# Kernel tuning notes

Hardware: AMD Instinct MI355X
Metric: run time of the kernel (lower is better)

The kernel has to match this reference:

```python
import jax, jax.numpy as jnp
import numpy as np

N_TOKENS = 8192
DIM = 7168
N_EXPERTS = 256
TOPK = 8
N_GROUPS = 8
TOPK_GROUPS = 4
ROUTE_SCALE = 2.5


def setup_inputs() -> dict:
    key = jax.random.key(0)
    k1, k2, k3 = jax.random.split(key, 3)
    x = jax.random.normal(k1, (N_TOKENS, DIM), jnp.float32)
    token_mask = jnp.ones((N_TOKENS,), jnp.bool_)
    weight = jax.random.normal(k2, (N_EXPERTS, DIM), jnp.float32) * 0.02
    bias = jax.random.normal(k3, (N_EXPERTS,), jnp.float32) * 0.01
    return {"x": x, "token_mask": token_mask, "weight": weight, "bias": bias}


def reference(x, token_mask, weight, bias):
    # Router logits -> sigmoid scores (DeepSeek-V3 style gate)
    N = x.shape[0]
    scores = jax.nn.sigmoid(jnp.einsum('nd,ed->ne', x, weight))  # [N, E]
    original_scores = scores
    # bias-corrected scores used only for expert selection
    s = scores + bias  # [N, E]
    # group-limited routing: pick TOPK_GROUPS groups by sum of top-2 scores per group
    sg = s.reshape(N, N_GROUPS, N_EXPERTS // N_GROUPS)
    group_scores = jax.lax.top_k(sg, 2)[0].sum(axis=-1)  # [N, G]
    group_idx = jax.lax.top_k(group_scores, TOPK_GROUPS)[1]  # [N, topk_groups]
    mask = jnp.zeros((N, N_GROUPS), s.dtype).at[jnp.arange(N)[:, None], group_idx].set(1.0)
    masked = (sg * mask[:, :, None]).reshape(N, N_EXPERTS)
    # global top-k over group-masked, bias-corrected scores
    idx = jax.lax.top_k(masked, TOPK)[1]  # [N, TOPK] int32
    # routing weights come from the ORIGINAL (un-biased) scores
    weights = jnp.take_along_axis(original_scores, idx, axis=1)  # [N, TOPK]
    # sigmoid score_func: renormalize then scale
    weights = weights / weights.sum(axis=-1, keepdims=True)
    weights = weights * ROUTE_SCALE
    return weights.astype(x.dtype), idx
```

## Files before the change

kernel.cpp:

```cpp
#include <hip/hip_runtime.h>
#include <math.h>

#define NT 8192
#define DIM 7168
#define NE 256

#define BM 64
#define BN 64
#define BK 16

__global__ __launch_bounds__(256) void gate_gemm_f64(const float* __restrict__ x,
                                                     const float* __restrict__ w,
                                                     double* __restrict__ scores) {
    __shared__ double As[BK][BM];
    __shared__ double Bs[BK][BN];
    const int eb = blockIdx.x;
    const int mb = blockIdx.y;
    const int t  = (int)threadIdx.x;
    const int lrow = t >> 2;
    const int kq   = (t & 3) << 2;
    const int ty = t >> 4;
    const int tx = t & 15;

    const float* ag = x + (size_t)(mb * BM + lrow) * DIM + kq;
    const float* bg = w + (size_t)(eb * BN + lrow) * DIM + kq;

    double acc[4][4];
    #pragma unroll
    for (int i = 0; i < 4; ++i)
        #pragma unroll
        for (int j = 0; j < 4; ++j) acc[i][j] = 0.0;

    float4 av = *(const float4*)ag;
    float4 bv = *(const float4*)bg;

    for (int kb = 0; kb < DIM; kb += BK) {
        __syncthreads();
        As[kq + 0][lrow] = (double)av.x; As[kq + 1][lrow] = (double)av.y;
        As[kq + 2][lrow] = (double)av.z; As[kq + 3][lrow] = (double)av.w;
        Bs[kq + 0][lrow] = (double)bv.x; Bs[kq + 1][lrow] = (double)bv.y;
        Bs[kq + 2][lrow] = (double)bv.z; Bs[kq + 3][lrow] = (double)bv.w;
        __syncthreads();
        if (kb + BK < DIM) {
            av = *(const float4*)(ag + kb + BK);
            bv = *(const float4*)(bg + kb + BK);
        }
        #pragma unroll
        for (int kk = 0; kk < BK; ++kk) {
            double ar[4], br[4];
            #pragma unroll
            for (int i = 0; i < 4; ++i) ar[i] = As[kk][i * 16 + ty];
            #pragma unroll
            for (int j = 0; j < 4; ++j) br[j] = Bs[kk][j * 16 + tx];
            #pragma unroll
            for (int i = 0; i < 4; ++i)
                #pragma unroll
                for (int j = 0; j < 4; ++j)
                    acc[i][j] = fma(ar[i], br[j], acc[i][j]);
        }
    }
    #pragma unroll
    for (int i = 0; i < 4; ++i) {
        const int m = mb * BM + i * 16 + ty;
        #pragma unroll
        for (int j = 0; j < 4; ++j) {
            const double s = 1.0 / (1.0 + exp(-acc[i][j]));
            scores[(size_t)m * NE + eb * BN + j * 16 + tx] = s;
        }
    }
}

__global__ __launch_bounds__(256) void gate_route_f64(const double* __restrict__ scores,
                                                      const float* __restrict__ bias,
                                                      float* __restrict__ out) {
    const int t = (int)threadIdx.x;
    const int lane = t & 63;
    const int token = blockIdx.x * 4 + (t >> 6);

    const double4 sc4 = *(const double4*)&scores[(size_t)token * NE + lane * 4];
    const float4 bi4 = *(const float4*)&bias[lane * 4];
    const double orig[4] = {sc4.x, sc4.y, sc4.z, sc4.w};
    const double sb[4] = {orig[0] + (double)bi4.x, orig[1] + (double)bi4.y,
                          orig[2] + (double)bi4.z, orig[3] + (double)bi4.w};

    const double m1 = fmax(sb[0], sb[1]), m2 = fmin(sb[0], sb[1]);
    const double m3 = fmax(sb[2], sb[3]), m4 = fmin(sb[2], sb[3]);
    double hi = fmax(m1, m3);
    double lo = fmax(fmin(m1, m3), fmax(m2, m4));
    #pragma unroll
    for (int off = 1; off < 8; off <<= 1) {
        const double oh = __shfl_xor(hi, off);
        const double ol = __shfl_xor(lo, off);
        const double nhi = fmax(hi, oh);
        const double nlo = fmax(fmin(hi, oh), fmax(lo, ol));
        hi = nhi; lo = nlo;
    }
    const double gsum = hi + lo;
    const int g = lane >> 3;

    int rank = 0;
    #pragma unroll
    for (int j = 0; j < 8; ++j) {
        const double gj = __shfl(gsum, j * 8);
        rank += (gj > gsum) || (gj == gsum && j < g);
    }
    const bool sel = rank < 4;

    double mv[4];
    #pragma unroll
    for (int i = 0; i < 4; ++i) mv[i] = sel ? sb[i] : 0.0;

    double wsel[8];
    int isel[8];
    double wsum = 0.0;
    #pragma unroll
    for (int r = 0; r < 8; ++r) {
        double v = mv[0]; int ii = 0;
        if (mv[1] > v) { v = mv[1]; ii = 1; }
        if (mv[2] > v) { v = mv[2]; ii = 2; }
        if (mv[3] > v) { v = mv[3]; ii = 3; }
        int idx = lane * 4 + ii;
        #pragma unroll
        for (int off = 1; off < 64; off <<= 1) {
            const double ov = __shfl_xor(v, off);
            const int    oi = __shfl_xor(idx, off);
            if (ov > v || (ov == v && oi < idx)) { v = ov; idx = oi; }
        }
        const int owner = idx >> 2, slot = idx & 3;
        const double os = (slot == 0) ? orig[0] : (slot == 1) ? orig[1]
                        : (slot == 2) ? orig[2] : orig[3];
        const double ow = __shfl(os, owner);
        wsel[r] = ow; isel[r] = idx; wsum += ow;
        if (lane == owner) {
            if      (slot == 0) mv[0] = -INFINITY;
            else if (slot == 1) mv[1] = -INFINITY;
            else if (slot == 2) mv[2] = -INFINITY;
            else                mv[3] = -INFINITY;
        }
    }

    if (lane == 0) {
        const double scale = 2.5 / wsum;
        #pragma unroll
        for (int r = 0; r < 8; ++r) {
            out[(size_t)token * 8 + r] = (float)(wsel[r] * scale);
            out[(size_t)NT * 8 + (size_t)token * 8 + r] = (float)isel[r];
        }
    }
}

extern "C" void kernel_launch(void* const* d_in, const int* in_sizes, int n_in,
                              void* d_out, int out_size, void* d_ws, size_t ws_size,
                              hipStream_t stream) {
    const float* x    = (const float*)d_in[0];
    const float* w    = (const float*)d_in[2];
    const float* bias = (const float*)d_in[3];
    float* out     = (float*)d_out;
    double* scores = (double*)d_ws;

    dim3 gGemm(NE / BN, NT / BM);
    gate_gemm_f64<<<gGemm, 256, 0, stream>>>(x, w, scores);
    gate_route_f64<<<NT / 4, 256, 0, stream>>>(scores, bias, out);
}
```

Measured before the change: 1.285 ms.

## Pre-transpose gate weights to f64 and read them via uniform broadcast loads

```diff
diff --git a/kernel.cpp b/kernel.cpp
--- a/kernel.cpp
+++ b/kernel.cpp
@@ -5,69 +5,78 @@
 #define DIM 7168
 #define NE 256
 
-#define BM 64
-#define BN 64
+#define TB 256
+#define TN 16
 #define BK 16
 
+
+__global__ __launch_bounds__(256) void wt_transpose(const float* __restrict__ w,
+                                                    double* __restrict__ wt) {
+    __shared__ float tile[32][33];
+    const int kb = blockIdx.x * 32;
+    const int eb = blockIdx.y * 32;
+    const int tx = (int)threadIdx.x & 31;
+    const int ty = (int)threadIdx.x >> 5;
+    #pragma unroll
+    for (int r = 0; r < 4; ++r)
+        tile[ty + r * 8][tx] = w[(size_t)(eb + ty + r * 8) * DIM + kb + tx];
+    __syncthreads();
+    #pragma unroll
+    for (int r = 0; r < 4; ++r)
+        wt[(size_t)(kb + ty + r * 8) * NE + eb + tx] = (double)tile[tx][ty + r * 8];
+}
+
 __global__ __launch_bounds__(256) void gate_gemm_f64(const float* __restrict__ x,
-                                                     const float* __restrict__ w,
+                                                     const double* __restrict__ wt,
                                                      double* __restrict__ scores) {
-    __shared__ double As[BK][BM];
-    __shared__ double Bs[BK][BN];
-    const int eb = blockIdx.x;
-    const int mb = blockIdx.y;
-    const int t  = (int)threadIdx.x;
-    const int lrow = t >> 2;
-    const int kq   = (t & 3) << 2;
-    const int ty = t >> 4;
-    const int tx = t & 15;
+    __shared__ double As[BK][TB];
+    const int tbk = blockIdx.x;
+    const int ebk = blockIdx.y;
+    const int t = (int)threadIdx.x;
+    const int ts = t >> 2;
+    const int kc = (t & 3) << 2;
 
-    const float* ag = x + (size_t)(mb * BM + lrow) * DIM + kq;
-    const float* bg = w + (size_t)(eb * BN + lrow) * DIM + kq;
+    const float* xg = x + (size_t)(tbk * TB) * DIM;
 
-    double acc[4][4];
+    double acc[TN];
     #pragma unroll
-    for (int i = 0; i < 4; ++i)
-        #pragma unroll
-        for (int j = 0; j < 4; ++j) acc[i][j] = 0.0;
+    for (int e = 0; e < TN; ++e) acc[e] = 0.0;
 
-    float4 av = *(const float4*)ag;
-    float4 bv = *(const float4*)bg;
+    float4 pv[4];
+    #pragma unroll
+    for (int r = 0; r < 4; ++r)
+        pv[r] = *(const float4*)(xg + (size_t)(ts + r * 64) * DIM + kc);
 
     for (int kb = 0; kb < DIM; kb += BK) {
         __syncthreads();
-        As[kq + 0][lrow] = (double)av.x; As[kq + 1][lrow] = (double)av.y;
-        As[kq + 2][lrow] = (double)av.z; As[kq + 3][lrow] = (double)av.w;
-        Bs[kq + 0][lrow] = (double)bv.x; Bs[kq + 1][lrow] = (double)bv.y;
-        Bs[kq + 2][lrow] = (double)bv.z; Bs[kq + 3][lrow] = (double)bv.w;
+        #pragma unroll
+        for (int r = 0; r < 4; ++r) {
+            const int tok = ts + r * 64;
+            As[kc + 0][tok] = (double)pv[r].x;
+            As[kc + 1][tok] = (double)pv[r].y;
+            As[kc + 2][tok] = (double)pv[r].z;
+            As[kc + 3][tok] = (double)pv[r].w;
+        }
         __syncthreads();
         if (kb + BK < DIM) {
-            av = *(const float4*)(ag + kb + BK);
-            bv = *(const float4*)(bg + kb + BK);
+            #pragma unroll
+            for (int r = 0; r < 4; ++r)
+                pv[r] = *(const float4*)(xg + (size_t)(ts + r * 64) * DIM + kb + BK + kc);
         }
-        #pragma unroll
+        const double* __restrict__ wrow = wt + (size_t)kb * NE + ebk * TN;
+        #pragma unroll 2
         for (int kk = 0; kk < BK; ++kk) {
-            double ar[4], br[4];
+            const double a = As[kk][t];
+            const double* __restrict__ br = wrow + (size_t)kk * NE;
             #pragma unroll
-            for (int i = 0; i < 4; ++i) ar[i] = As[kk][i * 16 + ty];
-            #pragma unroll
-            for (int j = 0; j < 4; ++j) br[j] = Bs[kk][j * 16 + tx];
-            #pragma unroll
-            for (int i = 0; i < 4; ++i)
-                #pragma unroll
-                for (int j = 0; j < 4; ++j)
-                    acc[i][j] = fma(ar[i], br[j], acc[i][j]);
+            for (int e = 0; e < TN; ++e)
+                acc[e] = fma(a, br[e], acc[e]);
         }
     }
+    double* srow = scores + (size_t)(tbk * TB + t) * NE + ebk * TN;
     #pragma unroll
-    for (int i = 0; i < 4; ++i) {
-        const int m = mb * BM + i * 16 + ty;
-        #pragma unroll
-        for (int j = 0; j < 4; ++j) {
-            const double s = 1.0 / (1.0 + exp(-acc[i][j]));
-            scores[(size_t)m * NE + eb * BN + j * 16 + tx] = s;
-        }
-    }
+    for (int e = 0; e < TN; ++e)
+        srow[e] = 1.0 / (1.0 + exp(-acc[e]));
 }
 
 __global__ __launch_bounds__(256) void gate_route_f64(const double* __restrict__ scores,
@@ -155,10 +164,12 @@
     const float* x    = (const float*)d_in[0];
     const float* w    = (const float*)d_in[2];
     const float* bias = (const float*)d_in[3];
-    float* out     = (float*)d_out;
-    double* scores = (double*)d_ws;
+    float* out = (float*)d_out;
 
-    dim3 gGemm(NE / BN, NT / BM);
-    gate_gemm_f64<<<gGemm, 256, 0, stream>>>(x, w, scores);
+    double* wt     = (double*)d_ws;
+    double* scores = wt + (size_t)DIM * NE;
+
+    wt_transpose<<<dim3(DIM / 32, NE / 32), 256, 0, stream>>>(w, wt);
+    gate_gemm_f64<<<dim3(NT / TB, NE / TN), 256, 0, stream>>>(x, wt, scores);
     gate_route_f64<<<NT / 4, 256, 0, stream>>>(scores, bias, out);
 }
```

Measured after the change: 1.808 ms. +40.7%, slower.
